# Kernel tuning notes

Measured on AMD Instinct MI355X. Metric: run time of the kernel, lower is better.

Reference implementation:

```python
import jax, jax.numpy as jnp
import numpy as np

CONF = 0.25
IOU = 0.7
MAX_DET = 300
IMG_H = 1280
IMG_W = 1280
KPT_SHAPE = (17, 3)
MAX_NMS = 3000
BS = 16
N_ANCH = 33600  # (1280/8)^2 + (1280/16)^2 + (1280/32)^2


def setup_inputs() -> dict:
    key = jax.random.key(0)
    k1, k2, k3, k4 = jax.random.split(key, 4)
    # realistic YOLO head outputs: centers in image, positive w/h, conf in (0,1)
    cxy = jax.random.uniform(k1, (BS, 2, N_ANCH)) * jnp.array([IMG_W, IMG_H], jnp.float32).reshape(1, 2, 1)
    wh = jax.random.uniform(k2, (BS, 2, N_ANCH)) * 200.0 + 4.0
    conf = jax.random.uniform(k3, (BS, 1, N_ANCH))
    kpts = jax.random.uniform(k4, (BS, 51, N_ANCH)) * float(IMG_W)
    preds = jnp.concatenate([cxy, wh, conf, kpts], axis=1).astype(jnp.float32)
    return {"preds": preds}


def _pairwise_iou(boxes):
    # boxes: [M, 4] xyxy
    area = (boxes[:, 2] - boxes[:, 0]) * (boxes[:, 3] - boxes[:, 1])
    lt = jnp.maximum(boxes[:, None, :2], boxes[None, :, :2])
    rb = jnp.minimum(boxes[:, None, 2:], boxes[None, :, 2:])
    wh = jnp.clip(rb - lt, 0.0)
    inter = wh[..., 0] * wh[..., 1]
    return inter / (area[:, None] + area[None, :] - inter + 1e-9)


def _nms_keep(boxes, valid):
    # greedy NMS over score-descending boxes; returns bool keep mask [M]
    M = boxes.shape[0]
    idx = jnp.arange(M)
    supp = (_pairwise_iou(boxes) > IOU) & (idx[None, :] > idx[:, None])

    def body(i, keep):
        # row i suppresses later boxes only if it is itself kept
        return keep & ~(supp[i] & keep[i])

    return jax.lax.fori_loop(0, M, body, valid)


def _per_image(boxes_xywh, scores, kpts):
    # boxes_xywh: [N,4], scores: [N], kpts: [N,51]
    valid = scores > CONF
    masked = jnp.where(valid, scores, -1.0)
    order = jnp.argsort(-masked)[:MAX_NMS]  # top max_nms by score, desc
    b = boxes_xywh[order]
    sc = scores[order]
    kp = kpts[order]
    v = valid[order]
    # xywh -> xyxy with clip to image bounds
    cx, cy, w, h = b[:, 0], b[:, 1], b[:, 2], b[:, 3]
    x1 = jnp.clip(cx - w / 2, 0.0, IMG_W)
    y1 = jnp.clip(cy - h / 2, 0.0, IMG_H)
    x2 = jnp.clip(cx + w / 2, 0.0, IMG_W)
    y2 = jnp.clip(cy + h / 2, 0.0, IMG_H)
    bxy = jnp.stack([x1, y1, x2, y2], axis=-1)
    # faithful to original _clip_coords quirk: only channels 0 and 1 of the 51 clipped
    kp = kp.at[:, 0].set(jnp.clip(kp[:, 0], 0.0, IMG_W))
    kp = kp.at[:, 1].set(jnp.clip(kp[:, 1], 0.0, IMG_H))
    keep = _nms_keep(bxy, v)
    rank = jnp.cumsum(keep) - 1
    sel = keep & (rank < MAX_DET)
    tgt = jnp.where(sel, rank, MAX_DET)  # dropped rows scatter to slot MAX_DET (sliced off)
    ob = jnp.zeros((MAX_DET + 1, 4), bxy.dtype).at[tgt].set(jnp.where(sel[:, None], bxy, 0.0))[:MAX_DET]
    osc = jnp.zeros((MAX_DET + 1, 1), sc.dtype).at[tgt].set(jnp.where(sel[:, None], sc[:, None], 0.0))[:MAX_DET]
    okp = jnp.zeros((MAX_DET + 1, 51), kp.dtype).at[tgt].set(jnp.where(sel[:, None], kp, 0.0))[:MAX_DET]
    return ob, osc, okp


def reference(preds):
    bs = preds.shape[0]
    x = jnp.transpose(preds, (0, 2, 1))  # [bs, N, 56]
    ob, osc, okp = jax.vmap(_per_image)(x[..., :4], x[..., 4], x[..., 5:])
    return ob, osc, okp.reshape(bs, MAX_DET, *KPT_SHAPE)
```

## Files before the change

### kernel.cpp

```cpp
#include <hip/hip_runtime.h>
#include <stdint.h>

#define N_ANCH 33600
#define BS 16
#define NCH 56
#define MAX_NMS 3000
#define MAX_DET 300
#define CONF_T 0.25f
#define IOU_T 0.7f
#define IMG 1280.0f
#define NW 47
#define NBINS 4096
#define HIST_BINS 4097
#define CAP 4096
#define WCAP 4096
#define WC_STRIDE 16
#define NIT 9
#define RNB 8

#define OFF_CAND 0
#define OFF_WL   (OFF_CAND + BS*CAP*8)
#define OFF_META (OFF_WL + BS*WCAP*4)
#define OFF_BOX  ((OFF_META + BS*MAX_NMS*8 + 15) & ~15)
#define OFF_WC   (OFF_BOX + BS*MAX_NMS*16)
#define OFF_GBM  (OFF_WC + BS*WC_STRIDE*4)
#define OFF_FOI  (OFF_GBM + BS*8)
#define OFF_DONE (OFF_FOI + BS*MAX_DET*4)

__device__ __forceinline__ int score_bucket(float c, uint32_t* bits_out) {
    if (!(c > CONF_T)) { *bits_out = 0u; return 0; }
    uint32_t bits = __float_as_uint(c);
    *bits_out = bits;
    int bucket = (int)(bits >> 12) - 0x3E800 + 1;
    bucket = bucket < 1 ? 1 : (bucket > NBINS ? NBINS : bucket);
    return bucket;
}

__device__ __forceinline__ float iou_pair(float4 bi, float ai, float4 bj) {
    float aj  = (bj.z - bj.x) * (bj.w - bj.y);
    float ltx = fmaxf(bi.x, bj.x), lty = fmaxf(bi.y, bj.y);
    float rbx = fminf(bi.z, bj.z), rby = fminf(bi.w, bj.w);
    float wx  = fmaxf(rbx - ltx, 0.f), wy = fmaxf(rby - lty, 0.f);
    float inter = wx * wy;
    return inter / (ai + aj - inter + 1e-9f);
}

__device__ __forceinline__ unsigned long long readlane64(unsigned long long v, int lane) {
    uint32_t lo = (uint32_t)v, hi = (uint32_t)(v >> 32);
    uint32_t rlo = __builtin_amdgcn_readlane(lo, lane);
    uint32_t rhi = __builtin_amdgcn_readlane(hi, lane);
    return ((unsigned long long)rhi << 32) | (unsigned long long)rlo;
}

__global__ void __launch_bounds__(1024)
k_phase1(const float* __restrict__ preds,
         unsigned long long* __restrict__ cand,
         unsigned int* __restrict__ wlist, int* __restrict__ wcount,
         int2* __restrict__ gbm, int* __restrict__ done) {
    __shared__ int hl[HIST_BINS];
    __shared__ int st[HIST_BINS];
    __shared__ int part[256];
    __shared__ int suf[256];
    __shared__ int ldsB, ldsM, ldsWc;
    const int b = blockIdx.x, t = threadIdx.x;
    if (t == 0) { ldsWc = 0; done[b] = 0; }
    for (int i = t; i < HIST_BINS; i += 1024) hl[i] = 0;
    __syncthreads();
    const float4* conf4 = (const float4*)(preds + (size_t)b * NCH * N_ANCH + 4 * N_ANCH);
    float4 rc[NIT];
    #pragma unroll
    for (int it = 0; it < NIT; it++) {
        int a4 = t + it * 1024;
        if (a4 < N_ANCH / 4) {
            float4 c4 = conf4[a4];
            rc[it] = c4;
            uint32_t bits;
            int bk;
            bk = score_bucket(c4.x, &bits); if (bk > 0) atomicAdd(&hl[bk], 1);
            bk = score_bucket(c4.y, &bits); if (bk > 0) atomicAdd(&hl[bk], 1);
            bk = score_bucket(c4.z, &bits); if (bk > 0) atomicAdd(&hl[bk], 1);
            bk = score_bucket(c4.w, &bits); if (bk > 0) atomicAdd(&hl[bk], 1);
        }
    }
    __syncthreads();
    if (t < 256) {
        int s = 0;
        for (int k = 0; k < 16; k++) s += hl[1 + t * 16 + k];
        part[t] = s;
    }
    __syncthreads();
    if (t < 64) {
        int p0 = part[4 * t + 0], p1 = part[4 * t + 1];
        int p2 = part[4 * t + 2], p3 = part[4 * t + 3];
        int loc = p0 + p1 + p2 + p3;
        int v = loc;
        #pragma unroll
        for (int off = 1; off < 64; off <<= 1) {
            int src = t + off;
            int o = __shfl(v, src & 63);
            if (src < 64) v += o;
        }
        int above = v - loc;
        suf[4 * t + 0] = above + p1 + p2 + p3;
        suf[4 * t + 1] = above + p2 + p3;
        suf[4 * t + 2] = above + p3;
        suf[4 * t + 3] = above;
        if (t == 0) {
            if (v < MAX_NMS) { ldsB = 1; ldsM = v; }
        }
    }
    __syncthreads();
    if (t < 256) {
        int run = suf[t];
        bool maycross = (run < MAX_NMS) && (run + part[t] >= MAX_NMS);
        bool done_ = false;
        for (int k = 15; k >= 0; k--) {
            int bin = 1 + t * 16 + k;
            st[bin] = run;
            run += hl[bin];
            if (maycross && !done_ && run >= MAX_NMS) { ldsB = bin; ldsM = run; done_ = true; }
        }
    }
    __syncthreads();
    const int B = ldsB;
    if (t < 256) {
        for (int k = 0; k < 16; k++) {
            int bin = 1 + t * 16 + k;
            int c = hl[bin], s = st[bin];
            if (c > 0 && bin >= B && s < MAX_NMS) {
                int idx = atomicAdd(&ldsWc, 1);
                wlist[b * WCAP + idx] = (unsigned int)s | ((unsigned int)c << 16);
            }
        }
    }
    __syncthreads();
    #pragma unroll
    for (int it = 0; it < NIT; it++) {
        int a4 = t + it * 1024;
        if (a4 < N_ANCH / 4) {
            float4 c4 = rc[it];
            float cv[4] = {c4.x, c4.y, c4.z, c4.w};
            #pragma unroll
            for (int q = 0; q < 4; q++) {
                uint32_t bits;
                int bucket = score_bucket(cv[q], &bits);
                if (bucket >= B && bucket > 0) {
                    int pos = atomicAdd(&st[bucket], 1);
                    if (pos < CAP) {
                        int a = a4 * 4 + q;
                        cand[b * CAP + pos] =
                            ((unsigned long long)bits << 32) | (uint32_t)(~(uint32_t)a);
                    }
                }
            }
        }
    }
    if (t == 0) {
        wcount[b * WC_STRIDE] = ldsWc;
        gbm[b] = make_int2(ldsB, ldsM);
    }
}

__global__ void __launch_bounds__(1024)
k_ranknms(const float* __restrict__ preds,
          const unsigned long long* __restrict__ cand,
          const unsigned int* __restrict__ wlist,
          const int* __restrict__ wcount,
          uint2* __restrict__ meta, float4* __restrict__ box_ws,
          const int2* __restrict__ gbm, int* __restrict__ done,
          int* __restrict__ foi, float* __restrict__ out) {
    __shared__ float4 lbox[MAX_NMS];
    __shared__ float4 kbox[MAX_DET];
    __shared__ float  karea[MAX_DET];
    __shared__ int    lsel[MAX_DET];
    __shared__ unsigned long long pres[NW];
    __shared__ unsigned long long diag[64];
    __shared__ unsigned long long keptmask_sh;
    __shared__ int lastFlag;
    const int b = blockIdx.x, t = threadIdx.x;
    {
        const int wc = wcount[b * WC_STRIDE];
        const int wv = blockIdx.y * 16 + (t >> 6);
        const int lane = t & 63;
        const float* pr = preds + (size_t)b * NCH * N_ANCH;
        for (int e = wv; e < wc; e += RNB * 16) {
            unsigned int ent = wlist[b * WCAP + e];
            int s = (int)(ent & 0xffffu);
            int n = (int)(ent >> 16);
            if (s + n > CAP) n = CAP - s;
            const unsigned long long* seg = cand + b * CAP + s;
            for (int i = lane; i < n; i += 64) {
                unsigned long long ke = seg[i];
                int r = 0;
                for (int j = 0; j < n; j++) r += (seg[j] > ke);
                int pos = s + r;
                if (pos < MAX_NMS) {
                    int oi = (int)(~(uint32_t)ke);
                    uint32_t sbits = (uint32_t)(ke >> 32);
                    float cx = pr[0 * N_ANCH + oi], cy = pr[1 * N_ANCH + oi];
                    float w  = pr[2 * N_ANCH + oi], h  = pr[3 * N_ANCH + oi];
                    float4 bx;
                    bx.x = fminf(fmaxf(cx - w * 0.5f, 0.f), IMG);
                    bx.y = fminf(fmaxf(cy - h * 0.5f, 0.f), IMG);
                    bx.z = fminf(fmaxf(cx + w * 0.5f, 0.f), IMG);
                    bx.w = fminf(fmaxf(cy + h * 0.5f, 0.f), IMG);
                    box_ws[b * MAX_NMS + pos] = bx;
                    meta[b * MAX_NMS + pos] = make_uint2((unsigned int)oi, sbits);
                }
            }
        }
    }
    __syncthreads();
    if (t == 0) {
        __threadfence();
        lastFlag = (atomicAdd(&done[b], 1) == RNB - 1);
    }
    __syncthreads();
    if (!lastFlag) return;
    if (t == 0) __threadfence();
    __syncthreads();

    const int M = gbm[b].y;
    const int Mc = M < MAX_NMS ? M : MAX_NMS;
    for (int j = t; j < Mc; j += 1024) lbox[j] = box_ws[b * MAX_NMS + j];
    if (t < NW) {
        int base = t * 64;
        int lo = Mc - base;
        unsigned long long inv = (lo <= 0) ? ~0ull : (lo >= 64 ? 0ull : ~((1ull << lo) - 1ull));
        pres[t] = inv;
    }
    __syncthreads();
    int kc = 0;
    const int nch = (Mc + 63) >> 6;
    for (int c = 0; c < nch && kc < MAX_DET; c++) {
        int base = c * 64;
        if (t < 64) diag[t] = 0ull;
        __syncthreads();
        {
            int jl = t >> 4, kk = t & 15;
            int j = base + jl;
            if (j < Mc && kc > 0) {
                float4 bj = lbox[j];
                bool sup = false;
                for (int kidx = kk; kidx < kc; kidx += 16) {
                    if (iou_pair(kbox[kidx], karea[kidx], bj) > IOU_T) { sup = true; break; }
                }
                if (sup) atomicOr(&pres[c], 1ull << jl);
            }
        }
        {
            int il = t >> 4;
            int j0 = (t & 15) * 4;
            int i = base + il;
            if (i < Mc) {
                float4 bi = lbox[i];
                float ai = (bi.z - bi.x) * (bi.w - bi.y);
                unsigned long long m = 0ull;
                for (int q = 0; q < 4; q++) {
                    int jl = j0 + q, j = base + jl;
                    if (j > i && j < Mc) {
                        if (iou_pair(bi, ai, lbox[j]) > IOU_T) m |= 1ull << jl;
                    }
                }
                if (m) atomicOr(&diag[il], m);
            }
        }
        __syncthreads();
        if (t < 64) {
            unsigned long long mydiag = diag[t];
            unsigned long long s = pres[c];
            unsigned long long keptm = 0ull;
            int room = MAX_DET - kc;
            int jmax = Mc - base; if (jmax > 64) jmax = 64;
            for (int bb = 0; bb < jmax; bb++) {
                if (!((s >> bb) & 1ull)) {
                    s |= readlane64(mydiag, bb);
                    keptm |= 1ull << bb;
                    if (--room == 0) break;
                }
            }
            if (t == 0) keptmask_sh = keptm;
        }
        __syncthreads();
        unsigned long long keptm = keptmask_sh;
        if (t < 64 && ((keptm >> t) & 1ull)) {
            int pos = kc + __popcll(keptm & ((1ull << t) - 1ull));
            float4 bx = lbox[base + t];
            kbox[pos] = bx;
            karea[pos] = (bx.z - bx.x) * (bx.w - bx.y);
            lsel[pos] = base + t;
        }
        kc += __popcll(keptm);
        __syncthreads();
    }
    float* ob  = out;
    float* osc = out + BS * MAX_DET * 4;
    for (int r = t; r < MAX_DET; r += 1024) {
        int det = b * MAX_DET + r;
        if (r < kc) {
            float4 bx = kbox[r];
            ob[det * 4 + 0] = bx.x; ob[det * 4 + 1] = bx.y;
            ob[det * 4 + 2] = bx.z; ob[det * 4 + 3] = bx.w;
            uint2 mt = meta[b * MAX_NMS + lsel[r]];
            osc[det] = __uint_as_float(mt.y);
            foi[det] = (int)mt.x;
        } else {
            ob[det * 4 + 0] = 0.f; ob[det * 4 + 1] = 0.f;
            ob[det * 4 + 2] = 0.f; ob[det * 4 + 3] = 0.f;
            osc[det] = 0.f;
            foi[det] = -1;
        }
    }
}

__global__ void k_kpt(const float* __restrict__ preds, const int* __restrict__ foi,
                      float* __restrict__ out) {
    int g = blockIdx.x * blockDim.x + threadIdx.x;
    if (g >= BS * MAX_DET * 51) return;
    int det = g / 51, lane = g - det * 51;
    int b = det / MAX_DET;
    float* okp = out + BS * MAX_DET * 5;
    int oi = foi[det];
    float v = 0.f;
    if (oi >= 0) {
        v = preds[(size_t)b * NCH * N_ANCH + (size_t)(5 + lane) * N_ANCH + oi];
        if (lane < 2) v = fminf(fmaxf(v, 0.f), IMG);
    }
    okp[g] = v;
}

extern "C" void kernel_launch(void* const* d_in, const int* in_sizes, int n_in,
                              void* d_out, int out_size, void* d_ws, size_t ws_size,
                              hipStream_t stream) {
    const float* preds = (const float*)d_in[0];
    float* out = (float*)d_out;
    char* ws = (char*)d_ws;
    unsigned long long* cand = (unsigned long long*)(ws + OFF_CAND);
    unsigned int* wlist = (unsigned int*)(ws + OFF_WL);
    uint2* meta = (uint2*)(ws + OFF_META);
    float4* box = (float4*)(ws + OFF_BOX);
    int* wcount = (int*)(ws + OFF_WC);
    int2* gbm = (int2*)(ws + OFF_GBM);
    int* foi = (int*)(ws + OFF_FOI);
    int* done = (int*)(ws + OFF_DONE);

    k_phase1<<<BS, 1024, 0, stream>>>(preds, cand, wlist, wcount, gbm, done);
    k_ranknms<<<dim3(BS, RNB), 1024, 0, stream>>>(preds, cand, wlist, wcount,
                                                  meta, box, gbm, done, foi, out);
    k_kpt<<<(BS * MAX_DET * 51 + 255) / 256, 256, 0, stream>>>(preds, foi, out);
}
```

Before: 230.2 us.

## Fuse rank into phase1, gather boxes lazily per NMS chunk

Moves the per-bucket rank sort into the histogram kernel, keeping the bucket worklist in LDS. The separate rank kernel with its 8 blocks per image, done-counter and threadfence handoff goes away. The NMS kernel now gathers box coordinates only for the 64-candidate chunk it is processing, so boxes past the point where 300 detections are found are never loaded. It also unrolls the rank comparison loop. In exchange, the rank work now runs on only 16 blocks instead of 128, which reduces parallelism, and each NMS chunk adds a dependent gather with an extra barrier.

```diff
diff --git a/kernel.cpp b/kernel.cpp
--- a/kernel.cpp
+++ b/kernel.cpp
@@ -13,19 +13,13 @@
 #define NBINS 4096
 #define HIST_BINS 4097
 #define CAP 4096
-#define WCAP 4096
-#define WC_STRIDE 16
+#define WLCAP 3072
 #define NIT 9
-#define RNB 8
 
 #define OFF_CAND 0
-#define OFF_WL   (OFF_CAND + BS*CAP*8)
-#define OFF_META (OFF_WL + BS*WCAP*4)
-#define OFF_BOX  ((OFF_META + BS*MAX_NMS*8 + 15) & ~15)
-#define OFF_WC   (OFF_BOX + BS*MAX_NMS*16)
-#define OFF_GBM  (OFF_WC + BS*WC_STRIDE*4)
+#define OFF_META (OFF_CAND + BS*CAP*8)
+#define OFF_GBM  (OFF_META + BS*MAX_NMS*8)
 #define OFF_FOI  (OFF_GBM + BS*8)
-#define OFF_DONE (OFF_FOI + BS*MAX_DET*4)
 
 __device__ __forceinline__ int score_bucket(float c, uint32_t* bits_out) {
     if (!(c > CONF_T)) { *bits_out = 0u; return 0; }
@@ -53,17 +47,17 @@
 }
 
 __global__ void __launch_bounds__(1024)
-k_phase1(const float* __restrict__ preds,
+k_p1rank(const float* __restrict__ preds,
          unsigned long long* __restrict__ cand,
-         unsigned int* __restrict__ wlist, int* __restrict__ wcount,
-         int2* __restrict__ gbm, int* __restrict__ done) {
+         uint2* __restrict__ meta, int2* __restrict__ gbm) {
     __shared__ int hl[HIST_BINS];
     __shared__ int st[HIST_BINS];
     __shared__ int part[256];
     __shared__ int suf[256];
+    __shared__ unsigned int wl[WLCAP];
     __shared__ int ldsB, ldsM, ldsWc;
     const int b = blockIdx.x, t = threadIdx.x;
-    if (t == 0) { ldsWc = 0; done[b] = 0; }
+    if (t == 0) ldsWc = 0;
     for (int i = t; i < HIST_BINS; i += 1024) hl[i] = 0;
     __syncthreads();
     const float4* conf4 = (const float4*)(preds + (size_t)b * NCH * N_ANCH + 4 * N_ANCH);
@@ -129,7 +123,8 @@
             int c = hl[bin], s = st[bin];
             if (c > 0 && bin >= B && s < MAX_NMS) {
                 int idx = atomicAdd(&ldsWc, 1);
-                wlist[b * WCAP + idx] = (unsigned int)s | ((unsigned int)c << 16);
+                if (idx < WLCAP)
+                    wl[idx] = (unsigned int)s | ((unsigned int)c << 16);
             }
         }
     }
@@ -155,74 +150,54 @@
             }
         }
     }
-    if (t == 0) {
-        wcount[b * WC_STRIDE] = ldsWc;
-        gbm[b] = make_int2(ldsB, ldsM);
-    }
-}
-
-__global__ void __launch_bounds__(1024)
-k_ranknms(const float* __restrict__ preds,
-          const unsigned long long* __restrict__ cand,
-          const unsigned int* __restrict__ wlist,
-          const int* __restrict__ wcount,
-          uint2* __restrict__ meta, float4* __restrict__ box_ws,
-          const int2* __restrict__ gbm, int* __restrict__ done,
-          int* __restrict__ foi, float* __restrict__ out) {
-    __shared__ float4 lbox[MAX_NMS];
-    __shared__ float4 kbox[MAX_DET];
-    __shared__ float  karea[MAX_DET];
-    __shared__ int    lsel[MAX_DET];
-    __shared__ unsigned long long pres[NW];
-    __shared__ unsigned long long diag[64];
-    __shared__ unsigned long long keptmask_sh;
-    __shared__ int lastFlag;
-    const int b = blockIdx.x, t = threadIdx.x;
+    __syncthreads();
     {
-        const int wc = wcount[b * WC_STRIDE];
-        const int wv = blockIdx.y * 16 + (t >> 6);
-        const int lane = t & 63;
-        const float* pr = preds + (size_t)b * NCH * N_ANCH;
-        for (int e = wv; e < wc; e += RNB * 16) {
-            unsigned int ent = wlist[b * WCAP + e];
+        const int wv = t >> 6, lane = t & 63;
+        int wc = ldsWc; if (wc > WLCAP) wc = WLCAP;
+        for (int e = wv; e < wc; e += 16) {
+            unsigned int ent = wl[e];
             int s = (int)(ent & 0xffffu);
             int n = (int)(ent >> 16);
             if (s + n > CAP) n = CAP - s;
             const unsigned long long* seg = cand + b * CAP + s;
             for (int i = lane; i < n; i += 64) {
                 unsigned long long ke = seg[i];
-                int r = 0;
-                for (int j = 0; j < n; j++) r += (seg[j] > ke);
+                int r = 0, j = 0;
+                for (; j + 8 <= n; j += 8) {
+                    unsigned long long k0 = seg[j + 0], k1 = seg[j + 1];
+                    unsigned long long k2 = seg[j + 2], k3 = seg[j + 3];
+                    unsigned long long k4 = seg[j + 4], k5 = seg[j + 5];
+                    unsigned long long k6 = seg[j + 6], k7 = seg[j + 7];
+                    r += (k0 > ke) + (k1 > ke) + (k2 > ke) + (k3 > ke)
+                       + (k4 > ke) + (k5 > ke) + (k6 > ke) + (k7 > ke);
+                }
+                for (; j < n; j++) r += (seg[j] > ke);
                 int pos = s + r;
-                if (pos < MAX_NMS) {
-                    int oi = (int)(~(uint32_t)ke);
-                    uint32_t sbits = (uint32_t)(ke >> 32);
-                    float cx = pr[0 * N_ANCH + oi], cy = pr[1 * N_ANCH + oi];
-                    float w  = pr[2 * N_ANCH + oi], h  = pr[3 * N_ANCH + oi];
-                    float4 bx;
-                    bx.x = fminf(fmaxf(cx - w * 0.5f, 0.f), IMG);
-                    bx.y = fminf(fmaxf(cy - h * 0.5f, 0.f), IMG);
-                    bx.z = fminf(fmaxf(cx + w * 0.5f, 0.f), IMG);
-                    bx.w = fminf(fmaxf(cy + h * 0.5f, 0.f), IMG);
-                    box_ws[b * MAX_NMS + pos] = bx;
-                    meta[b * MAX_NMS + pos] = make_uint2((unsigned int)oi, sbits);
-                }
-            }
-        }
-    }
-    __syncthreads();
-    if (t == 0) {
-        __threadfence();
-        lastFlag = (atomicAdd(&done[b], 1) == RNB - 1);
-    }
-    __syncthreads();
-    if (!lastFlag) return;
-    if (t == 0) __threadfence();
-    __syncthreads();
-
+                if (pos < MAX_NMS)
+                    meta[b * MAX_NMS + pos] =
+                        make_uint2(~(uint32_t)ke, (uint32_t)(ke >> 32));
+            }
+        }
+    }
+    if (t == 0) gbm[b] = make_int2(ldsB, ldsM);
+}
+
+__global__ void __launch_bounds__(1024)
+k_nms(const float* __restrict__ preds, const uint2* __restrict__ meta,
+      const int2* __restrict__ gbm, int* __restrict__ foi, float* __restrict__ out) {
+    __shared__ float  gbr[256];
+    __shared__ uint2  cmeta[64];
+    __shared__ float4 cb4[64];
+    __shared__ float4 kbox[MAX_DET];
+    __shared__ float  karea[MAX_DET];
+    __shared__ float  ksc[MAX_DET];
+    __shared__ int    koi[MAX_DET];
+    __shared__ unsigned long long pres[NW];
+    __shared__ unsigned long long diag[64];
+    __shared__ unsigned long long keptmask_sh;
+    const int b = blockIdx.x, t = threadIdx.x;
     const int M = gbm[b].y;
     const int Mc = M < MAX_NMS ? M : MAX_NMS;
-    for (int j = t; j < Mc; j += 1024) lbox[j] = box_ws[b * MAX_NMS + j];
     if (t < NW) {
         int base = t * 64;
         int lo = Mc - base;
@@ -232,15 +207,35 @@
     __syncthreads();
     int kc = 0;
     const int nch = (Mc + 63) >> 6;
+    const float* pr = preds + (size_t)b * NCH * N_ANCH;
     for (int c = 0; c < nch && kc < MAX_DET; c++) {
         int base = c * 64;
+        int jmax = Mc - base; if (jmax > 64) jmax = 64;
         if (t < 64) diag[t] = 0ull;
+        if (t < 256) {
+            int jl = t >> 2, q = t & 3;
+            if (jl < jmax) {
+                uint2 m = meta[b * MAX_NMS + base + jl];
+                if (q == 0) cmeta[jl] = m;
+                gbr[t] = pr[(size_t)q * N_ANCH + (int)m.x];
+            }
+        }
+        __syncthreads();
+        if (t < jmax) {
+            float cx = gbr[4 * t + 0], cy = gbr[4 * t + 1];
+            float w  = gbr[4 * t + 2], h  = gbr[4 * t + 3];
+            float4 bx;
+            bx.x = fminf(fmaxf(cx - w * 0.5f, 0.f), IMG);
+            bx.y = fminf(fmaxf(cy - h * 0.5f, 0.f), IMG);
+            bx.z = fminf(fmaxf(cx + w * 0.5f, 0.f), IMG);
+            bx.w = fminf(fmaxf(cy + h * 0.5f, 0.f), IMG);
+            cb4[t] = bx;
+        }
         __syncthreads();
         {
             int jl = t >> 4, kk = t & 15;
-            int j = base + jl;
-            if (j < Mc && kc > 0) {
-                float4 bj = lbox[j];
+            if (jl < jmax && kc > 0) {
+                float4 bj = cb4[jl];
                 bool sup = false;
                 for (int kidx = kk; kidx < kc; kidx += 16) {
                     if (iou_pair(kbox[kidx], karea[kidx], bj) > IOU_T) { sup = true; break; }
@@ -251,15 +246,14 @@
         {
             int il = t >> 4;
             int j0 = (t & 15) * 4;
-            int i = base + il;
-            if (i < Mc) {
-                float4 bi = lbox[i];
+            if (il < jmax) {
+                float4 bi = cb4[il];
                 float ai = (bi.z - bi.x) * (bi.w - bi.y);
                 unsigned long long m = 0ull;
                 for (int q = 0; q < 4; q++) {
-                    int jl = j0 + q, j = base + jl;
-                    if (j > i && j < Mc) {
-                        if (iou_pair(bi, ai, lbox[j]) > IOU_T) m |= 1ull << jl;
+                    int jl = j0 + q;
+                    if (jl > il && jl < jmax) {
+                        if (iou_pair(bi, ai, cb4[jl]) > IOU_T) m |= 1ull << jl;
                     }
                 }
                 if (m) atomicOr(&diag[il], m);
@@ -271,7 +265,6 @@
             unsigned long long s = pres[c];
             unsigned long long keptm = 0ull;
             int room = MAX_DET - kc;
-            int jmax = Mc - base; if (jmax > 64) jmax = 64;
             for (int bb = 0; bb < jmax; bb++) {
                 if (!((s >> bb) & 1ull)) {
                     s |= readlane64(mydiag, bb);
@@ -285,10 +278,11 @@
         unsigned long long keptm = keptmask_sh;
         if (t < 64 && ((keptm >> t) & 1ull)) {
             int pos = kc + __popcll(keptm & ((1ull << t) - 1ull));
-            float4 bx = lbox[base + t];
+            float4 bx = cb4[t];
             kbox[pos] = bx;
             karea[pos] = (bx.z - bx.x) * (bx.w - bx.y);
-            lsel[pos] = base + t;
+            koi[pos] = (int)cmeta[t].x;
+            ksc[pos] = __uint_as_float(cmeta[t].y);
         }
         kc += __popcll(keptm);
         __syncthreads();
@@ -301,9 +295,8 @@
             float4 bx = kbox[r];
             ob[det * 4 + 0] = bx.x; ob[det * 4 + 1] = bx.y;
             ob[det * 4 + 2] = bx.z; ob[det * 4 + 3] = bx.w;
-            uint2 mt = meta[b * MAX_NMS + lsel[r]];
-            osc[det] = __uint_as_float(mt.y);
-            foi[det] = (int)mt.x;
+            osc[det] = ksc[r];
+            foi[det] = koi[r];
         } else {
             ob[det * 4 + 0] = 0.f; ob[det * 4 + 1] = 0.f;
             ob[det * 4 + 2] = 0.f; ob[det * 4 + 3] = 0.f;
@@ -336,16 +329,11 @@
     float* out = (float*)d_out;
     char* ws = (char*)d_ws;
     unsigned long long* cand = (unsigned long long*)(ws + OFF_CAND);
-    unsigned int* wlist = (unsigned int*)(ws + OFF_WL);
     uint2* meta = (uint2*)(ws + OFF_META);
-    float4* box = (float4*)(ws + OFF_BOX);
-    int* wcount = (int*)(ws + OFF_WC);
     int2* gbm = (int2*)(ws + OFF_GBM);
     int* foi = (int*)(ws + OFF_FOI);
-    int* done = (int*)(ws + OFF_DONE);
-
-    k_phase1<<<BS, 1024, 0, stream>>>(preds, cand, wlist, wcount, gbm, done);
-    k_ranknms<<<dim3(BS, RNB), 1024, 0, stream>>>(preds, cand, wlist, wcount,
-                                                  meta, box, gbm, done, foi, out);
+
+    k_p1rank<<<BS, 1024, 0, stream>>>(preds, cand, meta, gbm);
+    k_nms<<<BS, 1024, 0, stream>>>(preds, meta, gbm, foi, out);
     k_kpt<<<(BS * MAX_DET * 51 + 255) / 256, 256, 0, stream>>>(preds, foi, out);
 }
```

After: 263.9 us. 1.15x slower.
